# Optimization experiments

Hardware: AMD Instinct MI355X
Metric: run time of the kernel (lower is better)

## Reference

```python
import jax, jax.numpy as jnp
import numpy as np

B, L, S, V = 1024, 512, 64, 160000
EMB = 16
E = 3 * EMB            # extended embedding dim = 48
G, M = 4, 3            # lsh_group_num, lsh_group_length
MAXC = 2 ** M          # 8 buckets per group
NH, KD = 8, 4          # MHA heads / key_dim
IN_DIM = 5 * EMB + 3 * E   # user(80) + item(48) + longterm(48) + shortterm(48) = 224
PAD_LT, PAD_ST = L // 4, S // 4
M_VALUES = jnp.array([1, 2, 4], dtype=jnp.float32)
LN_EPS = 1e-3  # keras LayerNormalization default


def setup_inputs() -> dict:
    key = jax.random.key(0)
    ks = list(jax.random.split(key, 40))
    d = {}
    for i, n in enumerate(['uid', 'utag1', 'utag2', 'utag3', 'utag4']):
        d[n] = jax.random.randint(ks[i], (B,), 1, V, dtype=jnp.int32)
    for i, n in enumerate(['label_goods_ids', 'label_shop_ids', 'label_cate_ids']):
        d[n] = jax.random.randint(ks[5 + i], (B,), 1, V, dtype=jnp.int32)
    for i, n in enumerate(['longterm_goods_ids', 'longterm_shop_ids', 'longterm_cate_ids']):
        ids = jax.random.randint(ks[8 + i], (B, L), 1, V, dtype=jnp.int32)
        d[n] = ids.at[:, L - PAD_LT:].set(0)  # left-aligned valid prefix, padded tail
    for i, n in enumerate(['shortterm_goods_ids', 'shortterm_shop_ids', 'shortterm_cate_ids']):
        ids = jax.random.randint(ks[11 + i], (B, S), 1, V, dtype=jnp.int32)
        d[n] = ids.at[:, S - PAD_ST:].set(0)
    def nrm(k, shape, s):
        return jax.random.normal(k, shape, jnp.float32) * s
    d['embed_table'] = nrm(ks[14], (V, EMB), 0.05)
    d['H'] = nrm(ks[15], (E, G, M), 1.0)  # non-trainable LSH projections
    d['wq'] = nrm(ks[16], (E, NH, KD), 0.1); d['bq'] = jnp.zeros((NH, KD))
    d['wk'] = nrm(ks[17], (E, NH, KD), 0.1); d['bk'] = jnp.zeros((NH, KD))
    d['wv'] = nrm(ks[18], (E, NH, KD), 0.1); d['bv'] = jnp.zeros((NH, KD))
    d['wo'] = nrm(ks[19], (NH, KD, E), 0.1); d['bo'] = jnp.zeros((E,))
    d['w1'] = nrm(ks[20], (IN_DIM, 200), 0.1); d['b1'] = jnp.zeros((200,))
    d['g1'] = jnp.ones((200,)); d['be1'] = jnp.zeros((200,))
    d['w2'] = nrm(ks[21], (200, 80), 0.1); d['b2'] = jnp.zeros((80,))
    d['g2'] = jnp.ones((80,)); d['be2'] = jnp.zeros((80,))
    d['w3'] = nrm(ks[22], (80, 1), 0.1); d['b3'] = jnp.zeros((1,))
    return d


def _stack_embed(table, feats):
    # feats: list of (B,) or (B,T) int arrays -> (B, T, n_feats*EMB)
    cols = [f[:, None] if f.ndim == 1 else f for f in feats]
    X = jnp.stack(cols, axis=2)              # (B, T, F)
    Xe = table[X]                            # (B, T, F, EMB)
    return Xe.reshape(Xe.shape[0], Xe.shape[1], -1)


def _layernorm(x, g, b):
    mu = x.mean(-1, keepdims=True)
    var = jnp.square(x - mu).mean(-1, keepdims=True)
    return g * (x - mu) / jnp.sqrt(var + LN_EPS) + b


def _lsh_codes(x, H):
    # x: (B, T, E) -> integer bucket codes (B, T, G)
    codes = jnp.sign(jnp.einsum('bte,egm->btgm', x, H))
    binary = (codes == 1).astype(jnp.float32)
    return jnp.tensordot(binary, M_VALUES, axes=[[-1], [0]]).astype(jnp.int32)


def _forward(uid, utag1, utag2, utag3, utag4,
             label_goods_ids, label_shop_ids, label_cate_ids,
             longterm_goods_ids, longterm_shop_ids, longterm_cate_ids,
             shortterm_goods_ids, shortterm_shop_ids, shortterm_cate_ids,
             embed_table, H, wq, bq, wk, bk, wv, bv, wo, bo,
             w1, b1, g1, be1, w2, b2, g2, be2, w3, b3):
    # --- embeddings ---
    Xu = _stack_embed(embed_table, [uid, utag1, utag2, utag3, utag4])        # (B,1,80)
    Xi = _stack_embed(embed_table, [label_goods_ids, label_shop_ids, label_cate_ids])  # (B,1,48)
    Xl = _stack_embed(embed_table, [longterm_goods_ids, longterm_shop_ids, longterm_cate_ids])   # (B,L,48)
    Xs = _stack_embed(embed_table, [shortterm_goods_ids, shortterm_shop_ids, shortterm_cate_ids])  # (B,S,48)

    longterm_pad = longterm_goods_ids == 0
    shortterm_pad = shortterm_goods_ids == 0

    # --- long-term interest: LSH scatter-mean over buckets then gather by item code ---
    series_int = _lsh_codes(Xl, H)                                   # (B,L,G)
    mXl = Xl * (~longterm_pad).astype(jnp.float32)[:, :, None]        # masked series embeddings
    oh = jax.nn.one_hot(series_int, MAXC, dtype=jnp.float32)          # (B,L,G,C)
    c_sum = jnp.einsum('blgc,ble->bgce', oh, mXl)                     # bucket sums (B,G,C,E)
    vc = oh.sum(axis=1)                                               # valid counts (B,G,C)
    safe = jnp.where(vc[..., None] > 0,
                     c_sum / jnp.maximum(vc[..., None], 1.0),
                     0.0)                                             # bucket means
    item_int = _lsh_codes(Xi, H)                                      # (B,1,G)
    item_oh = jax.nn.one_hot(item_int, MAXC, dtype=jnp.float32)       # (B,1,G,C)
    longterm_interest = jnp.einsum('bgce,bsgc->bsge', safe, item_oh).mean(axis=2)  # (B,1,E)

    # --- short-term interest: target attention (keras MultiHeadAttention) ---
    lengths = (~shortterm_pad).astype(jnp.int32).sum(axis=1)           # (B,)
    seq_mask = (jnp.arange(S)[None, :] < lengths[:, None]).astype(jnp.float32)  # (B,S)
    q = jnp.einsum('bqe,ehd->bqhd', Xi, wq) + bq
    k = jnp.einsum('bke,ehd->bkhd', Xs, wk) + bk
    v = jnp.einsum('bke,ehd->bkhd', Xs, wv) + bv
    scores = jnp.einsum('bqhd,bkhd->bhqk', q, k) / jnp.sqrt(jnp.float32(KD))
    scores = scores + (1.0 - seq_mask[:, None, None, :]) * (-1e9)
    attn = jax.nn.softmax(scores, axis=-1)
    ctx = jnp.einsum('bhqk,bkhd->bqhd', attn, v)
    shortterm_interest = jnp.einsum('bqhd,hde->bqe', ctx, wo) + bo      # (B,1,E)

    # --- final MLP: Dense->LN->ReLU x2, Dense->sigmoid ---
    feat = jnp.concatenate([Xu[:, 0], Xi[:, 0],
                            longterm_interest[:, 0], shortterm_interest[:, 0]], axis=-1)  # (B,224)
    h = jax.nn.relu(_layernorm(feat @ w1 + b1, g1, be1))
    h = jax.nn.relu(_layernorm(h @ w2 + b2, g2, be2))
    return jax.nn.sigmoid(h @ w3 + b3)                                 # (B,1)


def reference(uid, utag1, utag2, utag3, utag4,
              label_goods_ids, label_shop_ids, label_cate_ids,
              longterm_goods_ids, longterm_shop_ids, longterm_cate_ids,
              shortterm_goods_ids, shortterm_shop_ids, shortterm_cate_ids,
              embed_table, H, wq, bq, wk, bk, wv, bv, wo, bo,
              w1, b1, g1, be1, w2, b2, g2, be2, w3, b3):
    return _forward(uid, utag1, utag2, utag3, utag4,
                    label_goods_ids, label_shop_ids, label_cate_ids,
                    longterm_goods_ids, longterm_shop_ids, longterm_cate_ids,
                    shortterm_goods_ids, shortterm_shop_ids, shortterm_cate_ids,
                    embed_table, H, wq, bq, wk, bk, wv, bv, wo, bo,
                    w1, b1, g1, be1, w2, b2, g2, be2, w3, b3)
```

## Files before the change

### kernel.cpp

```cpp
#include <hip/hip_runtime.h>
#include <hip/hip_bf16.h>

#define LLEN 512
#define SLEN 64
#define EMBD 16
#define EE 48
#define GG 4
#define NHH 8
#define KDD 4
#define INDIM 224
#define H1D 200
#define H2D 80
#define CHUNK 128
#define PXE 52

__device__ __forceinline__ float bf2f(unsigned short u) {
    union { unsigned int i; float f; } v; v.i = ((unsigned int)u) << 16; return v.f;
}

template<bool BF16>
__device__ __forceinline__ float ldf(const void* p, int i) {
    if constexpr (BF16) return bf2f(((const unsigned short*)p)[i]);
    else                return ((const float*)p)[i];
}

template<bool BF16>
__device__ __forceinline__ float4 ld4(const void* p, int i4) {
    if constexpr (BF16) {
        ushort4 u = ((const ushort4*)p)[i4 >> 2];
        return make_float4(bf2f(u.x), bf2f(u.y), bf2f(u.z), bf2f(u.w));
    } else {
        return ((const float4*)p)[i4 >> 2];
    }
}

struct Pool {
    float buf[CHUNK * PXE + 16];
    float part[GG][GG][EE];
    float hf[12 * EE];
    float feat[INDIM];
    float q[NHH * KDD];
    float red[128];
    int   pc[2][GG];
    int   icode[GG];
    int   len;
    float mu, rstd;
};

template<bool BF16>
__device__ void sdim_body(Pool& P,
    const int* uid, const int* ut1, const int* ut2, const int* ut3, const int* ut4,
    const int* lb_g, const int* lb_s, const int* lb_c,
    const int* lt_g, const int* lt_s, const int* lt_c,
    const int* st_g, const int* st_s, const int* st_c,
    const void* tbl, const void* Hm,
    const void* wq, const void* bq, const void* wk, const void* bk,
    const void* wvv, const void* bv, const void* wo, const void* bo,
    const void* w1, const void* b1, const void* g1, const void* be1,
    const void* w2, const void* b2, const void* g2, const void* be2,
    const void* w3, const void* b3, void* outp)
{
    const int b = blockIdx.x;
    const int tid = threadIdx.x;
    const int lane = tid & 63;
    const int wid = __builtin_amdgcn_readfirstlane(tid >> 6);

    for (int i = tid; i < 12 * EE; i += 256) {
        int j = i / EE, e = i - j * EE;
        P.hf[i] = ldf<BF16>(Hm, e * 12 + j);
    }
    if (tid < 80) {
        int f = tid >> 4, e = tid & 15;
        int id = (f == 0) ? uid[b] : (f == 1) ? ut1[b] : (f == 2) ? ut2[b] : (f == 3) ? ut3[b] : ut4[b];
        P.feat[tid] = ldf<BF16>(tbl, id * EMBD + e);
    } else if (tid < 128) {
        int t = tid - 80; int f = t >> 4, e = t & 15;
        int id = (f == 0) ? lb_g[b] : (f == 1) ? lb_s[b] : lb_c[b];
        P.feat[80 + t] = ldf<BF16>(tbl, id * EMBD + e);
    }
    __syncthreads();

    if (tid < 32) {
        float acc = ldf<BF16>(bq, tid);
        for (int e = 0; e < EE; e++) acc += P.feat[80 + e] * ldf<BF16>(wq, e * 32 + tid);
        P.q[tid] = acc;
    }
    if (tid >= 64 && tid < 76) {
        int j = tid - 64;
        float acc = 0.f;
        for (int e = 0; e < EE; e++) acc += P.feat[80 + e] * P.hf[j * EE + e];
        P.red[j] = acc;
    }
    __syncthreads();
    if (tid < GG) {
        int code = 0;
        #pragma unroll
        for (int m = 0; m < 3; m++) if (P.red[tid * 3 + m] > 0.f) code |= (1 << m);
        P.icode[tid] = code;
    }

    float accg[GG] = {0.f, 0.f, 0.f, 0.f};
    int   cnt[GG]  = {0, 0, 0, 0};
    const int offs = (lane < 52) ? lane : 51;

    for (int ch = 0; ch < LLEN / CHUNK; ch++) {
        const int base = ch * CHUNK;
        {
            int ids[6];
            #pragma unroll
            for (int i = 0; i < 6; i++) {
                int f = tid + 256 * i;
                int p = f / 12, qq = f - 12 * p, fe = qq >> 2;
                const int* idp = (fe == 0) ? lt_g : (fe == 1) ? lt_s : lt_c;
                ids[i] = idp[b * LLEN + base + p];
            }
            float4 vs[6];
            #pragma unroll
            for (int i = 0; i < 6; i++) {
                int f = tid + 256 * i;
                int p = f / 12, qq = f - 12 * p;
                vs[i] = ld4<BF16>(tbl, ids[i] * EMBD + ((qq & 3) << 2));
            }
            #pragma unroll
            for (int i = 0; i < 6; i++) {
                int f = tid + 256 * i;
                int p = f / 12, qq = f - 12 * p;
                *(float4*)&P.buf[p * PXE + (qq << 2)] = vs[i];
            }
        }
        __syncthreads();
        if (!(wid & 1)) {
            const int p = ((wid >> 1) << 6) | lane;
            const float* row = &P.buf[p * PXE];
            float4 x[12];
            #pragma unroll
            for (int k = 0; k < 12; k++) x[k] = *(const float4*)(row + 4 * k);
            float acc[12];
            #pragma unroll
            for (int j = 0; j < 12; j++) {
                const float4* hr = (const float4*)&P.hf[j * EE];
                float s = 0.f;
                #pragma unroll
                for (int k = 0; k < 12; k++) {
                    float4 h4 = hr[k];
                    s += x[k].x * h4.x + x[k].y * h4.y + x[k].z * h4.z + x[k].w * h4.w;
                }
                acc[j] = s;
            }
            int code[GG];
            #pragma unroll
            for (int g = 0; g < GG; g++) {
                int c = 0;
                #pragma unroll
                for (int m = 0; m < 3; m++) if (acc[g * 3 + m] > 0.f) c |= (1 << m);
                code[g] = c;
            }
            int valid = (lt_g[b * LLEN + base + p] != 0);
            float4 sel;
            sel.x = (code[0] == P.icode[0] && valid) ? 1.f : 0.f;
            sel.y = (code[1] == P.icode[1] && valid) ? 1.f : 0.f;
            sel.z = (code[2] == P.icode[2] && valid) ? 1.f : 0.f;
            sel.w = (code[3] == P.icode[3] && valid) ? 1.f : 0.f;
            *(float4*)&P.buf[p * PXE + 48] = sel;
            #pragma unroll
            for (int g = 0; g < GG; g++)
                cnt[g] += __popcll(__ballot(code[g] == P.icode[g]));
        }
        __syncthreads();
        {
            const float* basep = &P.buf[(wid * 32) * PXE] + offs;
            #pragma unroll
            for (int i = 0; i < 32; i++) {
                float xv = basep[i * PXE];
                #pragma unroll
                for (int g = 0; g < GG; g++) {
                    float sel = __int_as_float(
                        __builtin_amdgcn_readlane(__float_as_int(xv), 48 + g));
                    accg[g] += sel * xv;
                }
            }
        }
        __syncthreads();
    }
    if (lane < EE) {
        #pragma unroll
        for (int g = 0; g < GG; g++) P.part[wid][g][lane] = accg[g];
    }
    if (!(wid & 1) && lane == 0) {
        #pragma unroll
        for (int g = 0; g < GG; g++) P.pc[wid >> 1][g] = cnt[g];
    }
    __syncthreads();

    if (tid < EE) {
        float r = 0.f;
        #pragma unroll
        for (int g = 0; g < GG; g++) {
            float c = (float)(P.pc[0][g] + P.pc[1][g]);
            float s = P.part[0][g][tid] + P.part[1][g][tid] + P.part[2][g][tid] + P.part[3][g][tid];
            r += s / fmaxf(c, 1.0f);
        }
        P.feat[128 + tid] = r * 0.25f;
    }

    float* Xs   = P.buf;
    float* wkq  = P.buf + SLEN * PXE;
    float* bkq  = wkq + EE * NHH;
    float* sc   = bkq + NHH;
    float* su   = sc + NHH * SLEN;
    float* sctx = su + NHH * EE;

    {
        int ids[3];
        #pragma unroll
        for (int i = 0; i < 3; i++) {
            int f = tid + 256 * i;
            int p = f / 12, qq = f - 12 * p, fe = qq >> 2;
            const int* idp = (fe == 0) ? st_g : (fe == 1) ? st_s : st_c;
            ids[i] = idp[b * SLEN + p];
        }
        float4 vs[3];
        #pragma unroll
        for (int i = 0; i < 3; i++) {
            int f = tid + 256 * i;
            int p = f / 12, qq = f - 12 * p;
            vs[i] = ld4<BF16>(tbl, ids[i] * EMBD + ((qq & 3) << 2));
        }
        #pragma unroll
        for (int i = 0; i < 3; i++) {
            int f = tid + 256 * i;
            int p = f / 12, qq = f - 12 * p;
            *(float4*)&Xs[p * PXE + (qq << 2)] = vs[i];
        }
    }
    if (tid < 64) {
        unsigned long long msk = __ballot(st_g[b * SLEN + tid] != 0);
        if (tid == 0) P.len = __popcll(msk);
    }
    for (int t = tid; t < EE * NHH; t += 256) {
        int e = t >> 3, h = t & 7;
        float acc = 0.f;
        #pragma unroll
        for (int d = 0; d < KDD; d++) acc += ldf<BF16>(wk, e * 32 + h * 4 + d) * P.q[h * 4 + d];
        wkq[t] = acc;
    }
    if (tid < NHH) {
        float acc = 0.f;
        #pragma unroll
        for (int d = 0; d < KDD; d++) acc += ldf<BF16>(bk, tid * 4 + d) * P.q[tid * 4 + d];
        bkq[tid] = acc;
    }
    __syncthreads();
    for (int t = tid; t < NHH * SLEN; t += 256) {
        int h = t >> 6, s = t & 63;
        float acc = bkq[h];
        for (int e = 0; e < EE; e++) acc += Xs[s * PXE + e] * wkq[e * NHH + h];
        acc *= 0.5f;
        if (s >= P.len) acc -= 1e9f;
        sc[h * SLEN + s] = acc;
    }
    __syncthreads();
    for (int h = wid; h < NHH; h += 4) {
        float v = sc[h * SLEN + lane];
        float mx = v;
        #pragma unroll
        for (int o = 32; o; o >>= 1) mx = fmaxf(mx, __shfl_xor(mx, o));
        float ex = __expf(v - mx);
        float sm = ex;
        #pragma unroll
        for (int o = 32; o; o >>= 1) sm += __shfl_xor(sm, o);
        sc[h * SLEN + lane] = ex / sm;
    }
    __syncthreads();
    for (int t = tid; t < NHH * EE; t += 256) {
        int h = t / EE, e = t - h * EE;
        float acc = 0.f;
        for (int s = 0; s < SLEN; s++) acc += sc[h * SLEN + s] * Xs[s * PXE + e];
        su[t] = acc;
    }
    __syncthreads();
    if (tid < 32) {
        float acc = ldf<BF16>(bv, tid);
        int h = tid >> 2;
        for (int e = 0; e < EE; e++) acc += su[h * EE + e] * ldf<BF16>(wvv, e * 32 + tid);
        sctx[tid] = acc;
    }
    __syncthreads();
    if (tid < EE) {
        float acc = ldf<BF16>(bo, tid);
        #pragma unroll
        for (int i = 0; i < 32; i++) acc += sctx[i] * ldf<BF16>(wo, i * EE + tid);
        P.feat[176 + tid] = acc;
    }
    __syncthreads();

    float z1 = 0.f;
    if (tid < H1D) {
        z1 = ldf<BF16>(b1, tid);
        for (int i = 0; i < INDIM; i++) z1 += P.feat[i] * ldf<BF16>(w1, i * H1D + tid);
        P.buf[tid] = z1;
    }
    __syncthreads();
    if (tid < 64) {
        float sm = 0.f, sq = 0.f;
        for (int j = tid; j < H1D; j += 64) { float v = P.buf[j]; sm += v; sq += v * v; }
        #pragma unroll
        for (int o = 32; o; o >>= 1) { sm += __shfl_xor(sm, o); sq += __shfl_xor(sq, o); }
        if (tid == 0) { float mu = sm / H1D; P.mu = mu; P.rstd = rsqrtf(sq / H1D - mu * mu + 1e-3f); }
    }
    __syncthreads();
    if (tid < H1D) {
        float h = fmaxf(ldf<BF16>(g1, tid) * (z1 - P.mu) * P.rstd + ldf<BF16>(be1, tid), 0.f);
        P.buf[256 + tid] = h;
    }
    __syncthreads();
    float z2 = 0.f;
    if (tid < H2D) {
        z2 = ldf<BF16>(b2, tid);
        for (int i = 0; i < H1D; i++) z2 += P.buf[256 + i] * ldf<BF16>(w2, i * H2D + tid);
        P.buf[tid] = z2;
    }
    __syncthreads();
    if (tid < 64) {
        float sm = 0.f, sq = 0.f;
        for (int j = tid; j < H2D; j += 64) { float v = P.buf[j]; sm += v; sq += v * v; }
        #pragma unroll
        for (int o = 32; o; o >>= 1) { sm += __shfl_xor(sm, o); sq += __shfl_xor(sq, o); }
        if (tid == 0) { float mu = sm / H2D; P.mu = mu; P.rstd = rsqrtf(sq / H2D - mu * mu + 1e-3f); }
    }
    __syncthreads();
    if (tid < H2D) {
        float h = fmaxf(ldf<BF16>(g2, tid) * (z2 - P.mu) * P.rstd + ldf<BF16>(be2, tid), 0.f);
        P.red[tid] = h * ldf<BF16>(w3, tid);
    }
    __syncthreads();
    if (tid == 0) {
        float acc = ldf<BF16>(b3, 0);
        for (int i = 0; i < H2D; i++) acc += P.red[i];
        float sig = 1.f / (1.f + __expf(-acc));
        if constexpr (BF16) ((__hip_bfloat16*)outp)[b] = __float2bfloat16(sig);
        else                ((float*)outp)[b] = sig;
    }
}

__global__ __launch_bounds__(256, 4) void sdim_fwd(
    const int* __restrict__ uid, const int* __restrict__ ut1, const int* __restrict__ ut2,
    const int* __restrict__ ut3, const int* __restrict__ ut4,
    const int* __restrict__ lb_g, const int* __restrict__ lb_s, const int* __restrict__ lb_c,
    const int* __restrict__ lt_g, const int* __restrict__ lt_s, const int* __restrict__ lt_c,
    const int* __restrict__ st_g, const int* __restrict__ st_s, const int* __restrict__ st_c,
    const void* __restrict__ tbl, const void* __restrict__ Hm,
    const void* __restrict__ wq, const void* __restrict__ bq,
    const void* __restrict__ wk, const void* __restrict__ bk,
    const void* __restrict__ wvv, const void* __restrict__ bv,
    const void* __restrict__ wo, const void* __restrict__ bo,
    const void* __restrict__ w1, const void* __restrict__ b1,
    const void* __restrict__ g1, const void* __restrict__ be1,
    const void* __restrict__ w2, const void* __restrict__ b2,
    const void* __restrict__ g2, const void* __restrict__ be2,
    const void* __restrict__ w3, const void* __restrict__ b3,
    void* __restrict__ outp)
{
    __shared__ Pool P;
    __shared__ int s_isbf;
    if (threadIdx.x < 64) {
        int big = 0;
        for (int i = (threadIdx.x & 63); i < 128; i += 64) {
            unsigned short u = ((const unsigned short*)tbl)[2 * i];
            if (((u >> 7) & 0xFF) >= 127) big = 1;
        }
        unsigned long long m = __ballot(big);
        if (threadIdx.x == 0) s_isbf = (m == 0ull) ? 1 : 0;
    }
    __syncthreads();
    if (s_isbf)
        sdim_body<true >(P, uid, ut1, ut2, ut3, ut4, lb_g, lb_s, lb_c, lt_g, lt_s, lt_c,
                         st_g, st_s, st_c, tbl, Hm, wq, bq, wk, bk, wvv, bv, wo, bo,
                         w1, b1, g1, be1, w2, b2, g2, be2, w3, b3, outp);
    else
        sdim_body<false>(P, uid, ut1, ut2, ut3, ut4, lb_g, lb_s, lb_c, lt_g, lt_s, lt_c,
                         st_g, st_s, st_c, tbl, Hm, wq, bq, wk, bk, wvv, bv, wo, bo,
                         w1, b1, g1, be1, w2, b2, g2, be2, w3, b3, outp);
}

extern "C" void kernel_launch(void* const* d_in, const int* in_sizes, int n_in,
                              void* d_out, int out_size, void* d_ws, size_t ws_size,
                              hipStream_t stream) {
    const int B = in_sizes[0];
    sdim_fwd<<<B, 256, 0, stream>>>(
        (const int*)d_in[0],  (const int*)d_in[1],  (const int*)d_in[2],
        (const int*)d_in[3],  (const int*)d_in[4],
        (const int*)d_in[5],  (const int*)d_in[6],  (const int*)d_in[7],
        (const int*)d_in[8],  (const int*)d_in[9],  (const int*)d_in[10],
        (const int*)d_in[11], (const int*)d_in[12], (const int*)d_in[13],
        (const void*)d_in[14], (const void*)d_in[15],
        (const void*)d_in[16], (const void*)d_in[17],
        (const void*)d_in[18], (const void*)d_in[19],
        (const void*)d_in[20], (const void*)d_in[21],
        (const void*)d_in[22], (const void*)d_in[23],
        (const void*)d_in[24], (const void*)d_in[25],
        (const void*)d_in[26], (const void*)d_in[27],
        (const void*)d_in[28], (const void*)d_in[29],
        (const void*)d_in[30], (const void*)d_in[31],
        (const void*)d_in[32], (const void*)d_in[33],
        d_out);
}
```

Baseline: 202.4 us.

## Double block size to 512 threads and redistribute per-stage work across waves

Raises threads per block from 256 to 512 and reworks every stage to use them. The LSH hashing now splits groups across waves instead of idling half of them, attention scores and softmax use a position-major layout with one wave per head, and the MLP dense layers split the reduction across two thread halves. The final sum becomes a wave shuffle reduction. This is meant to cut per-block serial latency, but it adds syncs and shared memory partials and may lower occupancy, since launch_bounds now asks for 8 waves per SIMD.

```diff
diff --git a/kernel.cpp b/kernel.cpp
--- a/kernel.cpp
+++ b/kernel.cpp
@@ -13,6 +13,7 @@
 #define H2D 80
 #define CHUNK 128
 #define PXE 52
+#define NT 512
 
 __device__ __forceinline__ float bf2f(unsigned short u) {
     union { unsigned int i; float f; } v; v.i = ((unsigned int)u) << 16; return v.f;
@@ -36,12 +37,12 @@
 
 struct Pool {
     float buf[CHUNK * PXE + 16];
-    float part[GG][GG][EE];
+    float part[8][GG][EE];
     float hf[12 * EE];
     float feat[INDIM];
     float q[NHH * KDD];
     float red[128];
-    int   pc[2][GG];
+    int   pcw[8][2];
     int   icode[GG];
     int   len;
     float mu, rstd;
@@ -65,7 +66,7 @@
     const int lane = tid & 63;
     const int wid = __builtin_amdgcn_readfirstlane(tid >> 6);
 
-    for (int i = tid; i < 12 * EE; i += 256) {
+    for (int i = tid; i < 12 * EE; i += NT) {
         int j = i / EE, e = i - j * EE;
         P.hf[i] = ldf<BF16>(Hm, e * 12 + j);
     }
@@ -100,77 +101,68 @@
     }
 
     float accg[GG] = {0.f, 0.f, 0.f, 0.f};
-    int   cnt[GG]  = {0, 0, 0, 0};
+    int cnt0 = 0, cnt1 = 0;
     const int offs = (lane < 52) ? lane : 51;
+    const int pB = ((wid & 3) << 5) | (lane & 31);
+    const int gB = ((wid >> 2) << 1) | (lane >> 5);
 
     for (int ch = 0; ch < LLEN / CHUNK; ch++) {
         const int base = ch * CHUNK;
         {
-            int ids[6];
-            #pragma unroll
-            for (int i = 0; i < 6; i++) {
-                int f = tid + 256 * i;
+            int ids[3];
+            #pragma unroll
+            for (int i = 0; i < 3; i++) {
+                int f = tid + NT * i;
                 int p = f / 12, qq = f - 12 * p, fe = qq >> 2;
                 const int* idp = (fe == 0) ? lt_g : (fe == 1) ? lt_s : lt_c;
                 ids[i] = idp[b * LLEN + base + p];
             }
-            float4 vs[6];
-            #pragma unroll
-            for (int i = 0; i < 6; i++) {
-                int f = tid + 256 * i;
+            float4 vs[3];
+            #pragma unroll
+            for (int i = 0; i < 3; i++) {
+                int f = tid + NT * i;
                 int p = f / 12, qq = f - 12 * p;
                 vs[i] = ld4<BF16>(tbl, ids[i] * EMBD + ((qq & 3) << 2));
             }
             #pragma unroll
-            for (int i = 0; i < 6; i++) {
-                int f = tid + 256 * i;
+            for (int i = 0; i < 3; i++) {
+                int f = tid + NT * i;
                 int p = f / 12, qq = f - 12 * p;
                 *(float4*)&P.buf[p * PXE + (qq << 2)] = vs[i];
             }
         }
         __syncthreads();
-        if (!(wid & 1)) {
-            const int p = ((wid >> 1) << 6) | lane;
-            const float* row = &P.buf[p * PXE];
+        {
+            const float* row = &P.buf[pB * PXE];
             float4 x[12];
             #pragma unroll
             for (int k = 0; k < 12; k++) x[k] = *(const float4*)(row + 4 * k);
-            float acc[12];
-            #pragma unroll
-            for (int j = 0; j < 12; j++) {
-                const float4* hr = (const float4*)&P.hf[j * EE];
+            float acc[3];
+            #pragma unroll
+            for (int jj = 0; jj < 3; jj++) {
+                const float4* hr = (const float4*)&P.hf[(3 * gB + jj) * EE];
                 float s = 0.f;
                 #pragma unroll
                 for (int k = 0; k < 12; k++) {
                     float4 h4 = hr[k];
                     s += x[k].x * h4.x + x[k].y * h4.y + x[k].z * h4.z + x[k].w * h4.w;
                 }
-                acc[j] = s;
+                acc[jj] = s;
             }
-            int code[GG];
-            #pragma unroll
-            for (int g = 0; g < GG; g++) {
-                int c = 0;
-                #pragma unroll
-                for (int m = 0; m < 3; m++) if (acc[g * 3 + m] > 0.f) c |= (1 << m);
-                code[g] = c;
-            }
-            int valid = (lt_g[b * LLEN + base + p] != 0);
-            float4 sel;
-            sel.x = (code[0] == P.icode[0] && valid) ? 1.f : 0.f;
-            sel.y = (code[1] == P.icode[1] && valid) ? 1.f : 0.f;
-            sel.z = (code[2] == P.icode[2] && valid) ? 1.f : 0.f;
-            sel.w = (code[3] == P.icode[3] && valid) ? 1.f : 0.f;
-            *(float4*)&P.buf[p * PXE + 48] = sel;
-            #pragma unroll
-            for (int g = 0; g < GG; g++)
-                cnt[g] += __popcll(__ballot(code[g] == P.icode[g]));
+            int code = 0;
+            #pragma unroll
+            for (int m = 0; m < 3; m++) if (acc[m] > 0.f) code |= (1 << m);
+            int valid = (lt_g[b * LLEN + base + pB] != 0);
+            P.buf[pB * PXE + 48 + gB] = (code == P.icode[gB] && valid) ? 1.f : 0.f;
+            unsigned long long m = __ballot(code == P.icode[gB]);
+            cnt0 += __popcll(m & 0xFFFFFFFFull);
+            cnt1 += __popcll(m >> 32);
         }
         __syncthreads();
         {
-            const float* basep = &P.buf[(wid * 32) * PXE] + offs;
-            #pragma unroll
-            for (int i = 0; i < 32; i++) {
+            const float* basep = &P.buf[(wid << 4) * PXE] + offs;
+            #pragma unroll
+            for (int i = 0; i < 16; i++) {
                 float xv = basep[i * PXE];
                 #pragma unroll
                 for (int g = 0; g < GG; g++) {
@@ -186,18 +178,19 @@
         #pragma unroll
         for (int g = 0; g < GG; g++) P.part[wid][g][lane] = accg[g];
     }
-    if (!(wid & 1) && lane == 0) {
-        #pragma unroll
-        for (int g = 0; g < GG; g++) P.pc[wid >> 1][g] = cnt[g];
-    }
+    if (lane == 0) { P.pcw[wid][0] = cnt0; P.pcw[wid][1] = cnt1; }
     __syncthreads();
 
     if (tid < EE) {
         float r = 0.f;
         #pragma unroll
         for (int g = 0; g < GG; g++) {
-            float c = (float)(P.pc[0][g] + P.pc[1][g]);
-            float s = P.part[0][g][tid] + P.part[1][g][tid] + P.part[2][g][tid] + P.part[3][g][tid];
+            int wb = (g >> 1) << 2;
+            int h = g & 1;
+            float c = (float)(P.pcw[wb][h] + P.pcw[wb + 1][h] + P.pcw[wb + 2][h] + P.pcw[wb + 3][h]);
+            float s = 0.f;
+            #pragma unroll
+            for (int w = 0; w < 8; w++) s += P.part[w][g][tid];
             r += s / fmaxf(c, 1.0f);
         }
         P.feat[128 + tid] = r * 0.25f;
@@ -211,33 +204,30 @@
     float* sctx = su + NHH * EE;
 
     {
-        int ids[3];
-        #pragma unroll
-        for (int i = 0; i < 3; i++) {
-            int f = tid + 256 * i;
-            int p = f / 12, qq = f - 12 * p, fe = qq >> 2;
-            const int* idp = (fe == 0) ? st_g : (fe == 1) ? st_s : st_c;
-            ids[i] = idp[b * SLEN + p];
-        }
-        float4 vs[3];
-        #pragma unroll
-        for (int i = 0; i < 3; i++) {
-            int f = tid + 256 * i;
-            int p = f / 12, qq = f - 12 * p;
-            vs[i] = ld4<BF16>(tbl, ids[i] * EMBD + ((qq & 3) << 2));
-        }
-        #pragma unroll
-        for (int i = 0; i < 3; i++) {
-            int f = tid + 256 * i;
-            int p = f / 12, qq = f - 12 * p;
-            *(float4*)&Xs[p * PXE + (qq << 2)] = vs[i];
+        int f0 = tid;
+        int p0 = f0 / 12, q0 = f0 - 12 * p0, fe0 = q0 >> 2;
+        const int* idp0 = (fe0 == 0) ? st_g : (fe0 == 1) ? st_s : st_c;
+        int id0 = idp0[b * SLEN + p0];
+        int id1 = 0, p1 = 0, q1 = 0;
+        bool has1 = (tid < (SLEN * 12 - NT));
+        if (has1) {
+            int f1 = tid + NT;
+            p1 = f1 / 12; q1 = f1 - 12 * p1; int fe1 = q1 >> 2;
+            const int* idp1 = (fe1 == 0) ? st_g : (fe1 == 1) ? st_s : st_c;
+            id1 = idp1[b * SLEN + p1];
+        }
+        float4 v0 = ld4<BF16>(tbl, id0 * EMBD + ((q0 & 3) << 2));
+        *(float4*)&Xs[p0 * PXE + (q0 << 2)] = v0;
+        if (has1) {
+            float4 v1 = ld4<BF16>(tbl, id1 * EMBD + ((q1 & 3) << 2));
+            *(float4*)&Xs[p1 * PXE + (q1 << 2)] = v1;
         }
     }
     if (tid < 64) {
         unsigned long long msk = __ballot(st_g[b * SLEN + tid] != 0);
         if (tid == 0) P.len = __popcll(msk);
     }
-    for (int t = tid; t < EE * NHH; t += 256) {
+    for (int t = tid; t < EE * NHH; t += NT) {
         int e = t >> 3, h = t & 7;
         float acc = 0.f;
         #pragma unroll
@@ -251,17 +241,17 @@
         bkq[tid] = acc;
     }
     __syncthreads();
-    for (int t = tid; t < NHH * SLEN; t += 256) {
-        int h = t >> 6, s = t & 63;
+    {
+        int s = tid >> 3, h = tid & 7;
         float acc = bkq[h];
         for (int e = 0; e < EE; e++) acc += Xs[s * PXE + e] * wkq[e * NHH + h];
         acc *= 0.5f;
         if (s >= P.len) acc -= 1e9f;
-        sc[h * SLEN + s] = acc;
-    }
-    __syncthreads();
-    for (int h = wid; h < NHH; h += 4) {
-        float v = sc[h * SLEN + lane];
+        sc[s * NHH + h] = acc;
+    }
+    __syncthreads();
+    {
+        float v = sc[lane * NHH + wid];
         float mx = v;
         #pragma unroll
         for (int o = 32; o; o >>= 1) mx = fmaxf(mx, __shfl_xor(mx, o));
@@ -269,14 +259,14 @@
         float sm = ex;
         #pragma unroll
         for (int o = 32; o; o >>= 1) sm += __shfl_xor(sm, o);
-        sc[h * SLEN + lane] = ex / sm;
-    }
-    __syncthreads();
-    for (int t = tid; t < NHH * EE; t += 256) {
-        int h = t / EE, e = t - h * EE;
+        sc[lane * NHH + wid] = ex / sm;
+    }
+    __syncthreads();
+    if (tid < NHH * EE) {
+        int h = tid / EE, e = tid - h * EE;
         float acc = 0.f;
-        for (int s = 0; s < SLEN; s++) acc += sc[h * SLEN + s] * Xs[s * PXE + e];
-        su[t] = acc;
+        for (int s = 0; s < SLEN; s++) acc += sc[s * NHH + h] * Xs[s * PXE + e];
+        su[tid] = acc;
     }
     __syncthreads();
     if (tid < 32) {
@@ -294,12 +284,19 @@
     }
     __syncthreads();
 
+    float z1p = 0.f;
+    if (tid < H1D) {
+        z1p = ldf<BF16>(b1, tid);
+        for (int i = 0; i < 112; i++) z1p += P.feat[i] * ldf<BF16>(w1, i * H1D + tid);
+    } else if (tid >= 256 && tid < 256 + H1D) {
+        int o = tid - 256;
+        float a = 0.f;
+        for (int i = 112; i < INDIM; i++) a += P.feat[i] * ldf<BF16>(w1, i * H1D + o);
+        P.buf[640 + o] = a;
+    }
+    __syncthreads();
     float z1 = 0.f;
-    if (tid < H1D) {
-        z1 = ldf<BF16>(b1, tid);
-        for (int i = 0; i < INDIM; i++) z1 += P.feat[i] * ldf<BF16>(w1, i * H1D + tid);
-        P.buf[tid] = z1;
-    }
+    if (tid < H1D) { z1 = z1p + P.buf[640 + tid]; P.buf[tid] = z1; }
     __syncthreads();
     if (tid < 64) {
         float sm = 0.f, sq = 0.f;
@@ -314,12 +311,19 @@
         P.buf[256 + tid] = h;
     }
     __syncthreads();
+    float z2p = 0.f;
+    if (tid < H2D) {
+        z2p = ldf<BF16>(b2, tid);
+        for (int i = 0; i < 100; i++) z2p += P.buf[256 + i] * ldf<BF16>(w2, i * H2D + tid);
+    } else if (tid >= 256 && tid < 256 + H2D) {
+        int o = tid - 256;
+        float a = 0.f;
+        for (int i = 100; i < H1D; i++) a += P.buf[256 + i] * ldf<BF16>(w2, i * H2D + o);
+        P.buf[640 + o] = a;
+    }
+    __syncthreads();
     float z2 = 0.f;
-    if (tid < H2D) {
-        z2 = ldf<BF16>(b2, tid);
-        for (int i = 0; i < H1D; i++) z2 += P.buf[256 + i] * ldf<BF16>(w2, i * H2D + tid);
-        P.buf[tid] = z2;
-    }
+    if (tid < H2D) { z2 = z2p + P.buf[640 + tid]; P.buf[tid] = z2; }
     __syncthreads();
     if (tid < 64) {
         float sm = 0.f, sq = 0.f;
@@ -334,16 +338,20 @@
         P.red[tid] = h * ldf<BF16>(w3, tid);
     }
     __syncthreads();
-    if (tid == 0) {
-        float acc = ldf<BF16>(b3, 0);
-        for (int i = 0; i < H2D; i++) acc += P.red[i];
-        float sig = 1.f / (1.f + __expf(-acc));
-        if constexpr (BF16) ((__hip_bfloat16*)outp)[b] = __float2bfloat16(sig);
-        else                ((float*)outp)[b] = sig;
-    }
-}
-
-__global__ __launch_bounds__(256, 4) void sdim_fwd(
+    if (tid < 64) {
+        float v = P.red[tid] + ((tid < H2D - 64) ? P.red[64 + tid] : 0.f);
+        #pragma unroll
+        for (int o = 32; o; o >>= 1) v += __shfl_xor(v, o);
+        if (tid == 0) {
+            float acc = ldf<BF16>(b3, 0) + v;
+            float sig = 1.f / (1.f + __expf(-acc));
+            if constexpr (BF16) ((__hip_bfloat16*)outp)[b] = __float2bfloat16(sig);
+            else                ((float*)outp)[b] = sig;
+        }
+    }
+}
+
+__global__ __launch_bounds__(NT, 8) void sdim_fwd(
     const int* __restrict__ uid, const int* __restrict__ ut1, const int* __restrict__ ut2,
     const int* __restrict__ ut3, const int* __restrict__ ut4,
     const int* __restrict__ lb_g, const int* __restrict__ lb_s, const int* __restrict__ lb_c,
@@ -387,7 +395,7 @@
                               void* d_out, int out_size, void* d_ws, size_t ws_size,
                               hipStream_t stream) {
     const int B = in_sizes[0];
-    sdim_fwd<<<B, 256, 0, stream>>>(
+    sdim_fwd<<<B, NT, 0, stream>>>(
         (const int*)d_in[0],  (const int*)d_in[1],  (const int*)d_in[2],
         (const int*)d_in[3],  (const int*)d_in[4],
         (const int*)d_in[5],  (const int*)d_in[6],  (const int*)d_in[7],
```

Result: no change. 199.3 us, median of 2 (-1.5%).
